# Performance work log

Measured on AMD Instinct MI355X. Metric: run time of the kernel, lower is better.

The kernel has to match this reference:

```python
import jax, jax.numpy as jnp
import numpy as np

N, E, IN_DIM, OUT_DIM = 50000, 800000, 128, 128
NEG_SLOPE = 0.01  # F.leaky_relu default


def gcn_conv(x, W, b, src, dst, n_nodes):
    """PyG GCNConv: symmetric norm with self-loops, linear (no bias) -> aggregate -> +bias.
    Self-loop contribution added analytically (norm = deg_inv_sqrt[i]^2) instead of
    materializing an extended edge list."""
    h = x @ W.T  # [N, out]
    deg = jnp.zeros((n_nodes,), x.dtype).at[dst].add(1.0) + 1.0  # in-degree incl. self-loop
    dis = jax.lax.rsqrt(deg)  # deg^{-1/2}
    norm = dis[src] * dis[dst]  # [E]
    msgs = h[src] * norm[:, None]  # gather + scale, [E, out]
    agg = jax.ops.segment_sum(msgs, dst, num_segments=n_nodes)  # scatter-add
    agg = agg + h * (dis * dis)[:, None]  # self-loop messages
    return agg + b


def setup_inputs() -> dict:
    key = jax.random.key(0)
    ks = jax.random.split(key, 6)
    x = jax.random.normal(ks[0], (N, IN_DIM), jnp.float32)
    edge_index = jax.random.randint(ks[1], (2, E), 0, N, dtype=jnp.int32)
    batch = jnp.zeros((N,), jnp.int32)
    W1 = jax.random.normal(ks[2], (OUT_DIM, IN_DIM), jnp.float32) * (1.0 / np.sqrt(IN_DIM))
    b1 = jnp.zeros((OUT_DIM,), jnp.float32)
    W2 = jax.random.normal(ks[3], (OUT_DIM, OUT_DIM), jnp.float32) * (1.0 / np.sqrt(OUT_DIM))
    b2 = jnp.zeros((OUT_DIM,), jnp.float32)
    return {"x": x, "edge_index": edge_index, "batch": batch,
            "W1": W1, "b1": b1, "W2": W2, "b2": b2}


def reference(x, edge_index, batch, W1, b1, W2, b2):
    src, dst = edge_index[0], edge_index[1]
    n = x.shape[0]
    h = gcn_conv(x, W1, b1, src, dst, n)
    h = jax.nn.leaky_relu(h, NEG_SLOPE)
    # dropout is identity in eval mode (training=False)
    return gcn_conv(h, W2, b2, src, dst, n)
```

## Files before the change

kernel.cpp:

```cpp
#include <hip/hip_runtime.h>
#include <hip/hip_bf16.h>
#include <hip/hip_fp16.h>

#define DIM 128
#define NCHUNK 256
#define XLD 136
#define WLD 136

typedef unsigned short u16;
typedef unsigned int u32;
typedef __attribute__((ext_vector_type(8))) short bf16x8;
typedef __attribute__((ext_vector_type(4))) float f32x4;

__device__ __forceinline__ float bfbits2f(u16 u) {
    return __uint_as_float(((u32)u) << 16);
}
__device__ __forceinline__ u16 f2bf(float f) {
    __hip_bfloat16 b = __float2bfloat16(f);
    return *reinterpret_cast<u16*>(&b);
}
__device__ __forceinline__ u32 pack2bf(float lo, float hi) {
    return (u32)f2bf(lo) | ((u32)f2bf(hi) << 16);
}
__device__ __forceinline__ float h16tof(u16 u) {
    __half hh = *reinterpret_cast<__half*>(&u);
    return __half2float(hh);
}
__device__ __forceinline__ u16 ftoh16(float f) {
    __half hh = __float2half(f);
    return *reinterpret_cast<u16*>(&hh);
}

__global__ void k_probe(const u16* __restrict__ x, int* __restrict__ flagp) {
    if (threadIdx.x == 0 && blockIdx.x == 0) {
        int weird = 0;
        for (int i = 0; i < 256; i += 2) {
            u16 v = x[i];
            int e = (v >> 7) & 0xff;
            if ((v & 0x7fff) != 0 && (e >= 133 || e <= 100)) weird++;
        }
        *flagp = (weird > 16) ? 1 : 0;
    }
}

__global__ __launch_bounds__(256) void k_count(const int* __restrict__ dst,
                                               int* __restrict__ counts,
                                               int* __restrict__ rank, int E) {
    int e = blockIdx.x * blockDim.x + threadIdx.x;
    if (e < E) rank[e] = atomicAdd(&counts[dst[e]], 1);
}

__global__ __launch_bounds__(256) void k_chunksum(const int* __restrict__ counts,
                                                  int* __restrict__ chunksum,
                                                  int N, int chunk) {
    __shared__ int r[256];
    int t = threadIdx.x, b = blockIdx.x;
    int idx = b * chunk + t;
    r[t] = (t < chunk && idx < N) ? counts[idx] : 0;
    __syncthreads();
    for (int off = 128; off > 0; off >>= 1) {
        if (t < off) r[t] += r[t + off];
        __syncthreads();
    }
    if (t == 0) chunksum[b] = r[0];
}

__global__ void k_scanbase(const int* __restrict__ chunksum,
                           int* __restrict__ chunkbase,
                           int* __restrict__ rowptr, int N) {
    if (threadIdx.x == 0 && blockIdx.x == 0) {
        int run = 0;
        for (int i = 0; i < NCHUNK; ++i) { chunkbase[i] = run; run += chunksum[i]; }
        rowptr[N] = run;
    }
}

__global__ __launch_bounds__(256) void k_rowptr(const int* __restrict__ counts,
                                                const int* __restrict__ chunkbase,
                                                int* __restrict__ rowptr,
                                                float* __restrict__ dis,
                                                u32* __restrict__ pay,
                                                int N, int chunk) {
    __shared__ int sc[256];
    int t = threadIdx.x, b = blockIdx.x;
    int idx = b * chunk + t;
    int v = (t < chunk && idx < N) ? counts[idx] : 0;
    sc[t] = v;
    __syncthreads();
    for (int off = 1; off < 256; off <<= 1) {
        int add = (t >= off) ? sc[t - off] : 0;
        __syncthreads();
        sc[t] += add;
        __syncthreads();
    }
    if (t < chunk && idx < N) {
        rowptr[idx] = chunkbase[b] + sc[t] - v;
        float dv = rsqrtf((float)v + 1.0f);
        dis[idx] = dv;
        pay[idx] = ((u32)idx << 16) | (u32)ftoh16(dv);
    }
}

__global__ __launch_bounds__(256) void k_fill(const int* __restrict__ src,
                                              const int* __restrict__ dst,
                                              const int* __restrict__ rowptr,
                                              const int* __restrict__ rank,
                                              const u32* __restrict__ pay,
                                              u32* __restrict__ elist, int E) {
    int e = blockIdx.x * blockDim.x + threadIdx.x;
    if (e < E) {
        int d = dst[e];
        int s = src[e];
        elist[rowptr[d] + rank[e]] = pay[s];
    }
}

__global__ __launch_bounds__(256) void k_gemm(const void* __restrict__ in,
                                              const void* __restrict__ W,
                                              u16* __restrict__ h, int N,
                                              const int* __restrict__ flagp, int in_mode) {
    __shared__ u16 Xs[64 * XLD];
    __shared__ u16 Wsh[128 * WLD];
    const int tid = threadIdx.x;
    const int flag = *flagp;
    const int in_f32 = in_mode ? flag : 0;
    const int n0 = blockIdx.x * 64;

    if (flag) {
        const float* Wf = (const float*)W;
        for (int t = tid; t < 128 * 32; t += 256) {
            int r = t >> 5, c4 = (t & 31) * 4;
            float4 w = *(const float4*)(Wf + r * DIM + c4);
            uint2 pw = make_uint2(pack2bf(w.x, w.y), pack2bf(w.z, w.w));
            *(uint2*)(Wsh + r * WLD + c4) = pw;
        }
    } else {
        const u16* Wu = (const u16*)W;
        for (int t = tid; t < 128 * 16; t += 256) {
            int r = t >> 4, c8 = (t & 15) * 8;
            *(int4*)(Wsh + r * WLD + c8) = *(const int4*)(Wu + r * DIM + c8);
        }
    }
    if (in_f32) {
        const float* xf = (const float*)in;
        for (int t = tid; t < 64 * 32; t += 256) {
            int r = t >> 5, c4 = (t & 31) * 4;
            int n = n0 + r;
            float4 xv = make_float4(0.f, 0.f, 0.f, 0.f);
            if (n < N) xv = *(const float4*)(xf + (size_t)n * DIM + c4);
            uint2 px = make_uint2(pack2bf(xv.x, xv.y), pack2bf(xv.z, xv.w));
            *(uint2*)(Xs + r * XLD + c4) = px;
        }
    } else {
        const u16* xu = (const u16*)in;
        for (int t = tid; t < 64 * 16; t += 256) {
            int r = t >> 4, c8 = (t & 15) * 8;
            int n = n0 + r;
            int4 v = make_int4(0, 0, 0, 0);
            if (n < N) v = *(const int4*)(xu + (size_t)n * DIM + c8);
            *(int4*)(Xs + r * XLD + c8) = v;
        }
    }
    __syncthreads();

    const int wid = tid >> 6;
    const int lane = tid & 63;
    const int m_base = wid * 16;
    const int idx16 = lane & 15;
    const int koff = (lane >> 4) * 8;

    bf16x8 afrag[4];
#pragma unroll
    for (int ks = 0; ks < 4; ++ks)
        afrag[ks] = *(const bf16x8*)(Xs + (m_base + idx16) * XLD + ks * 32 + koff);

    f32x4 acc[8];
#pragma unroll
    for (int ct = 0; ct < 8; ++ct) acc[ct] = (f32x4){0.f, 0.f, 0.f, 0.f};

#pragma unroll
    for (int ct = 0; ct < 8; ++ct) {
#pragma unroll
        for (int ks = 0; ks < 4; ++ks) {
            bf16x8 bfrag = *(const bf16x8*)(Wsh + (ct * 16 + idx16) * WLD + ks * 32 + koff);
            acc[ct] = __builtin_amdgcn_mfma_f32_16x16x32_bf16(afrag[ks], bfrag, acc[ct], 0, 0, 0);
        }
    }

    const int drow = (lane >> 4) * 4;
#pragma unroll
    for (int ct = 0; ct < 8; ++ct) {
#pragma unroll
        for (int r = 0; r < 4; ++r) {
            int row = n0 + m_base + drow + r;
            if (row < N) h[(size_t)row * DIM + ct * 16 + idx16] = f2bf(acc[ct][r]);
        }
    }
}

template <bool RELU, bool OUT_BF16>
__global__ __launch_bounds__(256) void k_agg(const u16* __restrict__ h,
                                             const float* __restrict__ dis,
                                             const int* __restrict__ rowptr,
                                             const u32* __restrict__ elist,
                                             const void* __restrict__ bias,
                                             void* __restrict__ out, int N,
                                             const int* __restrict__ flagp) {
    const int lane = threadIdx.x & 63;
    const int d = blockIdx.x * 4 + (threadIdx.x >> 6);
    if (d >= N) return;
    const int flag = *flagp;

    const int start = rowptr[d];
    const int end = rowptr[d + 1];
    const float dd = dis[d];

    float accA[8], accB[8];
#pragma unroll
    for (int k = 0; k < 8; ++k) { accA[k] = 0.f; accB[k] = 0.f; }

    int j = start;
    for (; j + 8 <= end; j += 8) {
        u32 ev[8];
#pragma unroll
        for (int k = 0; k < 8; ++k) ev[k] = elist[j + k];
        u32 hv[8];
#pragma unroll
        for (int k = 0; k < 8; ++k)
            hv[k] = *(const u32*)(h + ((size_t)(ev[k] >> 16)) * DIM + lane * 2);
#pragma unroll
        for (int k = 0; k < 8; ++k) {
            float w = h16tof((u16)(ev[k] & 0xffff));
            accA[k] = fmaf(bfbits2f((u16)(hv[k] & 0xffff)), w, accA[k]);
            accB[k] = fmaf(bfbits2f((u16)(hv[k] >> 16)), w, accB[k]);
        }
    }
    for (; j < end; ++j) {
        u32 e0 = elist[j];
        float w0 = h16tof((u16)(e0 & 0xffff));
        u32 u0 = *(const u32*)(h + ((size_t)(e0 >> 16)) * DIM + lane * 2);
        accA[0] = fmaf(bfbits2f((u16)(u0 & 0xffff)), w0, accA[0]);
        accB[0] = fmaf(bfbits2f((u16)(u0 >> 16)), w0, accB[0]);
    }
    float acc0 = ((accA[0] + accA[1]) + (accA[2] + accA[3])) +
                 ((accA[4] + accA[5]) + (accA[6] + accA[7]));
    float acc1 = ((accB[0] + accB[1]) + (accB[2] + accB[3])) +
                 ((accB[4] + accB[5]) + (accB[6] + accB[7]));
    acc0 *= dd;
    acc1 *= dd;
    {
        float d2 = dd * dd;
        u32 u = *(const u32*)(h + (size_t)d * DIM + lane * 2);
        acc0 = fmaf(bfbits2f((u16)(u & 0xffff)), d2, acc0);
        acc1 = fmaf(bfbits2f((u16)(u >> 16)), d2, acc1);
    }
    int c = lane * 2;
    float b0, b1;
    if (flag) {
        b0 = ((const float*)bias)[c];
        b1 = ((const float*)bias)[c + 1];
    } else {
        b0 = bfbits2f(((const u16*)bias)[c]);
        b1 = bfbits2f(((const u16*)bias)[c + 1]);
    }
    acc0 += b0;
    acc1 += b1;
    if (RELU) {
        acc0 = acc0 > 0.f ? acc0 : 0.01f * acc0;
        acc1 = acc1 > 0.f ? acc1 : 0.01f * acc1;
    }
    if (OUT_BF16) {
        u32 packed = (u32)f2bf(acc0) | ((u32)f2bf(acc1) << 16);
        *(u32*)((u16*)out + (size_t)d * DIM + c) = packed;
    } else {
        *(float2*)((float*)out + (size_t)d * DIM + c) = make_float2(acc0, acc1);
    }
}

extern "C" void kernel_launch(void* const* d_in, const int* in_sizes, int n_in,
                              void* d_out, int out_size, void* d_ws, size_t ws_size,
                              hipStream_t stream) {
    const void* x  = d_in[0];
    const int*  ei = (const int*)d_in[1];
    const void* W1 = d_in[3];
    const void* b1 = d_in[4];
    const void* W2 = d_in[5];
    const void* b2 = d_in[6];

    const int N = in_sizes[0] / DIM;
    const int E = in_sizes[1] / 2;
    const int* src = ei;
    const int* dst = ei + E;
    const int chunk = (N + NCHUNK - 1) / NCHUNK;

    char* ws = (char*)d_ws;
    size_t o = 0;
    int*   flagp    = (int*)(ws + o);   o += 256;
    float* dis      = (float*)(ws + o); o += (((size_t)N * 4 + 255) & ~(size_t)255);
    int*   counts   = (int*)(ws + o);   o += (((size_t)N * 4 + 255) & ~(size_t)255);
    int*   rowptr   = (int*)(ws + o);   o += (((size_t)(N + 1) * 4 + 255) & ~(size_t)255);
    u32*   pay      = (u32*)(ws + o);   o += (((size_t)N * 4 + 255) & ~(size_t)255);
    int*   chunksum = (int*)(ws + o);   o += 1024;
    int*   chunkbase= (int*)(ws + o);   o += 1024;
    int*   rank     = (int*)(ws + o);   o += (((size_t)E * 4 + 255) & ~(size_t)255);
    u32*   elist    = (u32*)(ws + o);   o += (((size_t)E * 4 + 255) & ~(size_t)255);
    u16*   h        = (u16*)(ws + o);

    const int eblk = (E + 255) / 256;
    const int gblk = (N + 63) / 64;
    const int ablk = (N + 3) / 4;

    k_probe<<<1, 64, 0, stream>>>((const u16*)x, flagp);
    hipMemsetAsync(counts, 0, (size_t)N * 4, stream);
    k_count<<<eblk, 256, 0, stream>>>(dst, counts, rank, E);
    k_chunksum<<<NCHUNK, 256, 0, stream>>>(counts, chunksum, N, chunk);
    k_scanbase<<<1, 64, 0, stream>>>(chunksum, chunkbase, rowptr, N);
    k_rowptr<<<NCHUNK, 256, 0, stream>>>(counts, chunkbase, rowptr, dis, pay, N, chunk);
    k_fill<<<eblk, 256, 0, stream>>>(src, dst, rowptr, rank, pay, elist, E);

    u16* act = (u16*)d_out;

    k_gemm<<<gblk, 256, 0, stream>>>(x, W1, h, N, flagp, 1);
    k_agg<true, true><<<ablk, 256, 0, stream>>>(h, dis, rowptr, elist, b1, act, N, flagp);

    k_gemm<<<gblk, 256, 0, stream>>>(act, W2, h, N, flagp, 0);
    k_agg<false, false><<<ablk, 256, 0, stream>>>(h, dis, rowptr, elist, b2, d_out, N, flagp);
}
```

Baseline: 269.7 us.

## Split aggregation by feature chunks with quarter-wave per node; fuse probe into count

New measurement: 287.0 us. 1.06x slower.

```diff
diff --git a/kernel.cpp b/kernel.cpp
--- a/kernel.cpp
+++ b/kernel.cpp
@@ -6,6 +6,7 @@
 #define NCHUNK 256
 #define XLD 136
 #define WLD 136
+#define AGG_NCH 4
 
 typedef unsigned short u16;
 typedef unsigned int u32;
@@ -31,8 +32,12 @@
     return *reinterpret_cast<u16*>(&hh);
 }
 
-__global__ void k_probe(const u16* __restrict__ x, int* __restrict__ flagp) {
-    if (threadIdx.x == 0 && blockIdx.x == 0) {
+__global__ __launch_bounds__(256) void k_count(const u16* __restrict__ x,
+                                               int* __restrict__ flagp,
+                                               const int* __restrict__ dst,
+                                               int* __restrict__ counts,
+                                               int* __restrict__ rank, int E) {
+    if (blockIdx.x == 0 && threadIdx.x == 0) {
         int weird = 0;
         for (int i = 0; i < 256; i += 2) {
             u16 v = x[i];
@@ -41,11 +46,6 @@
         }
         *flagp = (weird > 16) ? 1 : 0;
     }
-}
-
-__global__ __launch_bounds__(256) void k_count(const int* __restrict__ dst,
-                                               int* __restrict__ counts,
-                                               int* __restrict__ rank, int E) {
     int e = blockIdx.x * blockDim.x + threadIdx.x;
     if (e < E) rank[e] = atomicAdd(&counts[dst[e]], 1);
 }
@@ -204,12 +204,18 @@
                                              const int* __restrict__ rowptr,
                                              const u32* __restrict__ elist,
                                              const void* __restrict__ bias,
-                                             void* __restrict__ out, int N,
+                                             void* __restrict__ out, int N, int nb,
                                              const int* __restrict__ flagp) {
+    const int chunk = blockIdx.x / nb;
+    const int nblk  = blockIdx.x - chunk * nb;
     const int lane = threadIdx.x & 63;
-    const int d = blockIdx.x * 4 + (threadIdx.x >> 6);
+    const int wid  = threadIdx.x >> 6;
+    const int qd   = lane >> 4;
+    const int ql   = lane & 15;
+    const int d = nblk * 16 + wid * 4 + qd;
     if (d >= N) return;
     const int flag = *flagp;
+    const int c = chunk * 32 + ql * 2;
 
     const int start = rowptr[d];
     const int end = rowptr[d + 1];
@@ -227,7 +233,7 @@
         u32 hv[8];
 #pragma unroll
         for (int k = 0; k < 8; ++k)
-            hv[k] = *(const u32*)(h + ((size_t)(ev[k] >> 16)) * DIM + lane * 2);
+            hv[k] = *(const u32*)(h + ((size_t)(ev[k] >> 16)) * DIM + c);
 #pragma unroll
         for (int k = 0; k < 8; ++k) {
             float w = h16tof((u16)(ev[k] & 0xffff));
@@ -238,7 +244,7 @@
     for (; j < end; ++j) {
         u32 e0 = elist[j];
         float w0 = h16tof((u16)(e0 & 0xffff));
-        u32 u0 = *(const u32*)(h + ((size_t)(e0 >> 16)) * DIM + lane * 2);
+        u32 u0 = *(const u32*)(h + ((size_t)(e0 >> 16)) * DIM + c);
         accA[0] = fmaf(bfbits2f((u16)(u0 & 0xffff)), w0, accA[0]);
         accB[0] = fmaf(bfbits2f((u16)(u0 >> 16)), w0, accB[0]);
     }
@@ -250,11 +256,10 @@
     acc1 *= dd;
     {
         float d2 = dd * dd;
-        u32 u = *(const u32*)(h + (size_t)d * DIM + lane * 2);
+        u32 u = *(const u32*)(h + (size_t)d * DIM + c);
         acc0 = fmaf(bfbits2f((u16)(u & 0xffff)), d2, acc0);
         acc1 = fmaf(bfbits2f((u16)(u >> 16)), d2, acc1);
     }
-    int c = lane * 2;
     float b0, b1;
     if (flag) {
         b0 = ((const float*)bias)[c];
@@ -308,11 +313,11 @@
 
     const int eblk = (E + 255) / 256;
     const int gblk = (N + 63) / 64;
-    const int ablk = (N + 3) / 4;
-
-    k_probe<<<1, 64, 0, stream>>>((const u16*)x, flagp);
+    const int nb   = (N + 15) / 16;
+    const int ablk = nb * AGG_NCH;
+
     hipMemsetAsync(counts, 0, (size_t)N * 4, stream);
-    k_count<<<eblk, 256, 0, stream>>>(dst, counts, rank, E);
+    k_count<<<eblk, 256, 0, stream>>>((const u16*)x, flagp, dst, counts, rank, E);
     k_chunksum<<<NCHUNK, 256, 0, stream>>>(counts, chunksum, N, chunk);
     k_scanbase<<<1, 64, 0, stream>>>(chunksum, chunkbase, rowptr, N);
     k_rowptr<<<NCHUNK, 256, 0, stream>>>(counts, chunkbase, rowptr, dis, pay, N, chunk);
@@ -321,8 +326,8 @@
     u16* act = (u16*)d_out;
 
     k_gemm<<<gblk, 256, 0, stream>>>(x, W1, h, N, flagp, 1);
-    k_agg<true, true><<<ablk, 256, 0, stream>>>(h, dis, rowptr, elist, b1, act, N, flagp);
+    k_agg<true, true><<<ablk, 256, 0, stream>>>(h, dis, rowptr, elist, b1, act, N, nb, flagp);
 
     k_gemm<<<gblk, 256, 0, stream>>>(act, W2, h, N, flagp, 0);
-    k_agg<false, false><<<ablk, 256, 0, stream>>>(h, dis, rowptr, elist, b2, d_out, N, flagp);
-}
+    k_agg<false, false><<<ablk, 256, 0, stream>>>(h, dis, rowptr, elist, b2, d_out, N, nb, flagp);
+}
```

## Vectorize aggregation gathers to 16B per lane with four edges per wavefront step

Applied to the files above, without the earlier changes.

Result: faster. 252.0 us (-6.5%).

```diff
diff --git a/kernel.cpp b/kernel.cpp
--- a/kernel.cpp
+++ b/kernel.cpp
@@ -31,8 +31,12 @@
     return *reinterpret_cast<u16*>(&hh);
 }
 
-__global__ void k_probe(const u16* __restrict__ x, int* __restrict__ flagp) {
-    if (threadIdx.x == 0 && blockIdx.x == 0) {
+__global__ __launch_bounds__(256) void k_count(const u16* __restrict__ x,
+                                               int* __restrict__ flagp,
+                                               const int* __restrict__ dst,
+                                               int* __restrict__ counts,
+                                               int* __restrict__ rank, int E) {
+    if (blockIdx.x == 0 && threadIdx.x == 0) {
         int weird = 0;
         for (int i = 0; i < 256; i += 2) {
             u16 v = x[i];
@@ -41,11 +45,6 @@
         }
         *flagp = (weird > 16) ? 1 : 0;
     }
-}
-
-__global__ __launch_bounds__(256) void k_count(const int* __restrict__ dst,
-                                               int* __restrict__ counts,
-                                               int* __restrict__ rank, int E) {
     int e = blockIdx.x * blockDim.x + threadIdx.x;
     if (e < E) rank[e] = atomicAdd(&counts[dst[e]], 1);
 }
@@ -210,70 +209,82 @@
     const int d = blockIdx.x * 4 + (threadIdx.x >> 6);
     if (d >= N) return;
     const int flag = *flagp;
+    const int q  = lane >> 4;
+    const int cb = (lane & 15) * 8;
 
     const int start = rowptr[d];
-    const int end = rowptr[d + 1];
-    const float dd = dis[d];
-
-    float accA[8], accB[8];
-#pragma unroll
-    for (int k = 0; k < 8; ++k) { accA[k] = 0.f; accB[k] = 0.f; }
-
-    int j = start;
-    for (; j + 8 <= end; j += 8) {
-        u32 ev[8];
-#pragma unroll
-        for (int k = 0; k < 8; ++k) ev[k] = elist[j + k];
-        u32 hv[8];
-#pragma unroll
-        for (int k = 0; k < 8; ++k)
-            hv[k] = *(const u32*)(h + ((size_t)(ev[k] >> 16)) * DIM + lane * 2);
-#pragma unroll
-        for (int k = 0; k < 8; ++k) {
-            float w = h16tof((u16)(ev[k] & 0xffff));
-            accA[k] = fmaf(bfbits2f((u16)(hv[k] & 0xffff)), w, accA[k]);
-            accB[k] = fmaf(bfbits2f((u16)(hv[k] >> 16)), w, accB[k]);
-        }
-    }
-    for (; j < end; ++j) {
-        u32 e0 = elist[j];
-        float w0 = h16tof((u16)(e0 & 0xffff));
-        u32 u0 = *(const u32*)(h + ((size_t)(e0 >> 16)) * DIM + lane * 2);
-        accA[0] = fmaf(bfbits2f((u16)(u0 & 0xffff)), w0, accA[0]);
-        accB[0] = fmaf(bfbits2f((u16)(u0 >> 16)), w0, accB[0]);
-    }
-    float acc0 = ((accA[0] + accA[1]) + (accA[2] + accA[3])) +
-                 ((accA[4] + accA[5]) + (accA[6] + accA[7]));
-    float acc1 = ((accB[0] + accB[1]) + (accB[2] + accB[3])) +
-                 ((accB[4] + accB[5]) + (accB[6] + accB[7]));
-    acc0 *= dd;
-    acc1 *= dd;
-    {
-        float d2 = dd * dd;
-        u32 u = *(const u32*)(h + (size_t)d * DIM + lane * 2);
-        acc0 = fmaf(bfbits2f((u16)(u & 0xffff)), d2, acc0);
-        acc1 = fmaf(bfbits2f((u16)(u >> 16)), d2, acc1);
-    }
-    int c = lane * 2;
-    float b0, b1;
+    const int end   = rowptr[d + 1];
+    const int last  = end - 1;
+    const float dd  = dis[d];
+
+    float acc[8];
+#pragma unroll
+    for (int k = 0; k < 8; ++k) acc[k] = 0.f;
+
+    for (int j = start; j < end; j += 8) {
+        int i0 = j + q;
+        int i1 = j + 4 + q;
+        u32 e0 = elist[i0 <= last ? i0 : last];
+        u32 e1 = elist[i1 <= last ? i1 : last];
+        float w0 = (i0 <= last) ? h16tof((u16)(e0 & 0xffff)) : 0.f;
+        float w1 = (i1 <= last) ? h16tof((u16)(e1 & 0xffff)) : 0.f;
+        const int4* p0 = (const int4*)(h + ((size_t)(e0 >> 16)) * DIM + cb);
+        const int4* p1 = (const int4*)(h + ((size_t)(e1 >> 16)) * DIM + cb);
+        int4 r0 = *p0;
+        int4 r1 = *p1;
+        u32 v0[4] = {(u32)r0.x, (u32)r0.y, (u32)r0.z, (u32)r0.w};
+        u32 v1[4] = {(u32)r1.x, (u32)r1.y, (u32)r1.z, (u32)r1.w};
+#pragma unroll
+        for (int k = 0; k < 4; ++k) {
+            acc[2 * k]     = fmaf(bfbits2f((u16)(v0[k] & 0xffff)), w0, acc[2 * k]);
+            acc[2 * k + 1] = fmaf(bfbits2f((u16)(v0[k] >> 16)),    w0, acc[2 * k + 1]);
+        }
+#pragma unroll
+        for (int k = 0; k < 4; ++k) {
+            acc[2 * k]     = fmaf(bfbits2f((u16)(v1[k] & 0xffff)), w1, acc[2 * k]);
+            acc[2 * k + 1] = fmaf(bfbits2f((u16)(v1[k] >> 16)),    w1, acc[2 * k + 1]);
+        }
+    }
+
+#pragma unroll
+    for (int k = 0; k < 8; ++k) {
+        acc[k] += __shfl_xor(acc[k], 16, 64);
+        acc[k] += __shfl_xor(acc[k], 32, 64);
+    }
+
+    if (q != 0) return;
+
+    const float d2 = dd * dd;
+    int4 rs = *(const int4*)(h + (size_t)d * DIM + cb);
+    u32 vs[4] = {(u32)rs.x, (u32)rs.y, (u32)rs.z, (u32)rs.w};
+    float res[8];
+#pragma unroll
+    for (int k = 0; k < 4; ++k) {
+        res[2 * k]     = fmaf(bfbits2f((u16)(vs[k] & 0xffff)), d2, acc[2 * k] * dd);
+        res[2 * k + 1] = fmaf(bfbits2f((u16)(vs[k] >> 16)),    d2, acc[2 * k + 1] * dd);
+    }
     if (flag) {
-        b0 = ((const float*)bias)[c];
-        b1 = ((const float*)bias)[c + 1];
+        const float* bf = (const float*)bias;
+#pragma unroll
+        for (int k = 0; k < 8; ++k) res[k] += bf[cb + k];
     } else {
-        b0 = bfbits2f(((const u16*)bias)[c]);
-        b1 = bfbits2f(((const u16*)bias)[c + 1]);
-    }
-    acc0 += b0;
-    acc1 += b1;
+        const u16* bu = (const u16*)bias;
+#pragma unroll
+        for (int k = 0; k < 8; ++k) res[k] += bfbits2f(bu[cb + k]);
+    }
     if (RELU) {
-        acc0 = acc0 > 0.f ? acc0 : 0.01f * acc0;
-        acc1 = acc1 > 0.f ? acc1 : 0.01f * acc1;
+#pragma unroll
+        for (int k = 0; k < 8; ++k) res[k] = res[k] > 0.f ? res[k] : 0.01f * res[k];
     }
     if (OUT_BF16) {
-        u32 packed = (u32)f2bf(acc0) | ((u32)f2bf(acc1) << 16);
-        *(u32*)((u16*)out + (size_t)d * DIM + c) = packed;
+        u32 pk[4];
+#pragma unroll
+        for (int k = 0; k < 4; ++k) pk[k] = pack2bf(res[2 * k], res[2 * k + 1]);
+        *(int4*)((u16*)out + (size_t)d * DIM + cb) = make_int4(pk[0], pk[1], pk[2], pk[3]);
     } else {
-        *(float2*)((float*)out + (size_t)d * DIM + c) = make_float2(acc0, acc1);
+        float* op = (float*)out + (size_t)d * DIM + cb;
+        *(float4*)op       = make_float4(res[0], res[1], res[2], res[3]);
+        *(float4*)(op + 4) = make_float4(res[4], res[5], res[6], res[7]);
     }
 }
 
@@ -310,9 +321,8 @@
     const int gblk = (N + 63) / 64;
     const int ablk = (N + 3) / 4;
 
-    k_probe<<<1, 64, 0, stream>>>((const u16*)x, flagp);
     hipMemsetAsync(counts, 0, (size_t)N * 4, stream);
-    k_count<<<eblk, 256, 0, stream>>>(dst, counts, rank, E);
+    k_count<<<eblk, 256, 0, stream>>>((const u16*)x, flagp, dst, counts, rank, E);
     k_chunksum<<<NCHUNK, 256, 0, stream>>>(counts, chunksum, N, chunk);
     k_scanbase<<<1, 64, 0, stream>>>(chunksum, chunkbase, rowptr, N);
     k_rowptr<<<NCHUNK, 256, 0, stream>>>(counts, chunkbase, rowptr, dis, pay, N, chunk);
```
